# Kernel optimization log

Measured on AMD Instinct MI355X. Metric: run time of the kernel, lower is better.

Reference implementation:

```python
import jax, jax.numpy as jnp
import numpy as np

N, F_IN, HEADS, F_OUT = 4096, 128, 4, 32
DENSITY = 0.05


def setup_inputs() -> dict:
    key = jax.random.key(0)
    k_x, k_adj, k_w, k_as, k_ad, k_b = jax.random.split(key, 6)
    x = jax.random.normal(k_x, (N, F_IN), dtype=jnp.float32)
    # binary adjacency with self-loops so every row of Tau_sum is nonzero
    adj = (jax.random.uniform(k_adj, (N, N)) < DENSITY).astype(jnp.float32)
    adj = jnp.maximum(adj, jnp.eye(N, dtype=jnp.float32))
    weight = jax.random.normal(k_w, (HEADS * F_OUT, F_IN), dtype=jnp.float32) * 0.1
    att_src = jax.random.normal(k_as, (1, HEADS, F_OUT), dtype=jnp.float32) * 0.1
    att_dst = jax.random.normal(k_ad, (1, HEADS, F_OUT), dtype=jnp.float32) * 0.1
    bias = jax.random.normal(k_b, (HEADS * F_OUT,), dtype=jnp.float32) * 0.1
    return {"x": x, "adj_matrix": adj, "weight": weight,
            "att_src": att_src, "att_dst": att_dst, "bias": bias}


def reference(x, adj_matrix, weight, att_src, att_dst, bias):
    n = x.shape[0]
    heads = att_src.shape[1]
    f_out = weight.shape[0] // heads
    # H' = x W^T, reshaped to [N, heads, F_out]
    h_prime = (x @ weight.T).reshape(n, heads, f_out)
    alpha_src = jnp.sum(h_prime * att_src, axis=-1)  # [N, heads]
    alpha_dst = jnp.sum(h_prime * att_dst, axis=-1)  # [N, heads]
    # C[m, n, h] = alpha_src[n, h] + alpha_dst[m, h]
    C = alpha_src[None, :, :] + alpha_dst[:, None, :]
    adj_t = adj_matrix.T[..., None]                  # [N, N, 1]
    # exp(leaky_relu(C, 0.2)) masked by adjacency
    tau = adj_t * jnp.exp(jnp.maximum(0.2 * C, C))   # [N, N, heads]
    tau_sum = jnp.sum(tau, axis=1, keepdims=True)    # [N, 1, heads]
    att_weights = tau / tau_sum
    # Z[m, h, f] = sum_n (adjT * att)[m, n, h] * H'[n, h, f]
    z = jnp.einsum('mnh,nhf->mhf', adj_t * att_weights, h_prime)
    return z.reshape(n, heads * f_out) + bias
```

## Files before the change

kernel.cpp:

```cpp
#include <hip/hip_runtime.h>

#define N_NODES 4096
#define F_IN    128
#define HEADS   4
#define FTOT    128
#define CAP     512
#define LCAP    40

__global__ __launch_bounds__(128)
void k_hp(const float* __restrict__ x, const float* __restrict__ W,
          const float* __restrict__ att_src, const float* __restrict__ att_dst,
          float* __restrict__ hp, float* __restrict__ as_, float* __restrict__ ad_,
          int* __restrict__ cnt)
{
    const int b  = blockIdx.x;
    const int t  = threadIdx.x;
    const int i0 = b * 4;
    if (t < 4) cnt[i0 + t] = 0;
    __shared__ float xs[4 * F_IN];
    reinterpret_cast<float4*>(xs)[t] =
        reinterpret_cast<const float4*>(x + (size_t)i0 * F_IN)[t];
    __syncthreads();

    const float4* W4  = reinterpret_cast<const float4*>(W + t * F_IN);
    const float4* xs4 = reinterpret_cast<const float4*>(xs);
    float a0 = 0.f, a1 = 0.f, a2 = 0.f, a3 = 0.f;
#pragma unroll
    for (int k = 0; k < F_IN / 4; ++k) {
        const float4 w  = W4[k];
        const float4 v0 = xs4[k], v1 = xs4[32 + k], v2 = xs4[64 + k], v3 = xs4[96 + k];
        a0 = fmaf(w.x, v0.x, a0); a0 = fmaf(w.y, v0.y, a0); a0 = fmaf(w.z, v0.z, a0); a0 = fmaf(w.w, v0.w, a0);
        a1 = fmaf(w.x, v1.x, a1); a1 = fmaf(w.y, v1.y, a1); a1 = fmaf(w.z, v1.z, a1); a1 = fmaf(w.w, v1.w, a1);
        a2 = fmaf(w.x, v2.x, a2); a2 = fmaf(w.y, v2.y, a2); a2 = fmaf(w.z, v2.z, a2); a2 = fmaf(w.w, v2.w, a2);
        a3 = fmaf(w.x, v3.x, a3); a3 = fmaf(w.y, v3.y, a3); a3 = fmaf(w.z, v3.z, a3); a3 = fmaf(w.w, v3.w, a3);
    }
    hp[(size_t)(i0 + 0) * FTOT + t] = a0;
    hp[(size_t)(i0 + 1) * FTOT + t] = a1;
    hp[(size_t)(i0 + 2) * FTOT + t] = a2;
    hp[(size_t)(i0 + 3) * FTOT + t] = a3;

    const float asv = att_src[t], adv = att_dst[t];
    float s0 = a0 * asv, s1 = a1 * asv, s2 = a2 * asv, s3 = a3 * asv;
    float d0 = a0 * adv, d1 = a1 * adv, d2 = a2 * adv, d3 = a3 * adv;
#pragma unroll
    for (int s = 16; s; s >>= 1) {
        s0 += __shfl_xor(s0, s); s1 += __shfl_xor(s1, s);
        s2 += __shfl_xor(s2, s); s3 += __shfl_xor(s3, s);
        d0 += __shfl_xor(d0, s); d1 += __shfl_xor(d1, s);
        d2 += __shfl_xor(d2, s); d3 += __shfl_xor(d3, s);
    }
    if ((t & 31) == 0) {
        const int hh = t >> 5;
        as_[(i0 + 0) * HEADS + hh] = s0; as_[(i0 + 1) * HEADS + hh] = s1;
        as_[(i0 + 2) * HEADS + hh] = s2; as_[(i0 + 3) * HEADS + hh] = s3;
        ad_[(i0 + 0) * HEADS + hh] = d0; ad_[(i0 + 1) * HEADS + hh] = d1;
        ad_[(i0 + 2) * HEADS + hh] = d2; ad_[(i0 + 3) * HEADS + hh] = d3;
    }
}

__global__ __launch_bounds__(256)
void k_scan(const float* __restrict__ adj, int* __restrict__ cnt,
            unsigned short* __restrict__ lists)
{
    __shared__ int lcnt[64];
    __shared__ int gbase[64];
    __shared__ unsigned short lbuf[64][LCAP];
    const int t     = threadIdx.x;
    const int strip = blockIdx.x & 63;
    const int chunk = blockIdx.x >> 6;
    const int c0    = strip * 64;
    const int r0    = chunk * 128;
    const int q     = t & 15;
    const int p     = t >> 4;
    if (t < 64) lcnt[t] = 0;
    __syncthreads();

    const float4* adj4 = reinterpret_cast<const float4*>(adj);
    float4 v[8];
#pragma unroll
    for (int it = 0; it < 8; ++it)
        v[it] = adj4[(size_t)(r0 + p + it * 16) * (N_NODES / 4) + (c0 >> 2) + q];

    unsigned mk0 = 0, mk1 = 0, mk2 = 0, mk3 = 0;
#pragma unroll
    for (int it = 0; it < 8; ++it) {
        mk0 |= (v[it].x != 0.f) ? (1u << it) : 0u;
        mk1 |= (v[it].y != 0.f) ? (1u << it) : 0u;
        mk2 |= (v[it].z != 0.f) ? (1u << it) : 0u;
        mk3 |= (v[it].w != 0.f) ? (1u << it) : 0u;
    }
    unsigned mks[4] = {mk0, mk1, mk2, mk3};
#pragma unroll
    for (int j = 0; j < 4; ++j) {
        unsigned mask = mks[j];
        if (mask) {
            const int ml = 4 * q + j;
            int slot = atomicAdd(&lcnt[ml], __popc(mask));
            while (mask) {
                const int it = __ffs(mask) - 1;
                mask &= mask - 1;
                lbuf[ml][slot++] = (unsigned short)(r0 + p + it * 16);
            }
        }
    }
    __syncthreads();
    if (t < 64) gbase[t] = atomicAdd(&cnt[c0 + t], lcnt[t]);
    __syncthreads();
    const int ml  = t >> 2;
    const int sub = t & 3;
    const int nn  = lcnt[ml];
    unsigned short* dst = lists + (size_t)(c0 + ml) * CAP + gbase[ml];
    for (int j = sub; j < nn; j += 4) dst[j] = lbuf[ml][j];
}

__global__ __launch_bounds__(256)
void k_agg(const float* __restrict__ hp, const float* __restrict__ as_,
           const float* __restrict__ ad_, const int* __restrict__ cnt,
           const unsigned short* __restrict__ lists,
           const float* __restrict__ bias, float* __restrict__ out)
{
    __shared__ float e_s[4][64][4];
    __shared__ float mrg[2][32][5];
    const int t    = threadIdx.x;
    const int wv   = t >> 6;
    const int ms   = wv >> 1;
    const int wp   = wv & 1;
    const int l    = t & 63;
    const int m    = blockIdx.x * 2 + ms;
    const int half = l >> 5;
    const int l32  = l & 31;
    const int h    = l32 >> 3;

    const int2 c2   = reinterpret_cast<const int2*>(cnt)[blockIdx.x];
    const int  cm   = ms ? c2.y : c2.x;
    const int  chalf = (cm + 1) >> 1;
    const int  begin = wp ? chalf : 0;
    const int  end   = wp ? cm : chalf;

    const float4 adm = reinterpret_cast<const float4*>(ad_)[m];
    const unsigned short* lst = lists + (size_t)m * CAP;
    const float4* hp4 = reinterpret_cast<const float4*>(hp);
    const float4* as4 = reinterpret_cast<const float4*>(as_);

    float4 acc = make_float4(0.f, 0.f, 0.f, 0.f);
    float tau = 0.f;

    const int nbat = (end - begin + 63) >> 6;
    for (int b = 0; b < nbat; ++b) {
        const int k0 = begin + b * 64;
        const bool valid = (k0 + l) < end;
        const int myidx = valid ? (int)lst[k0 + l] : 0;
        const float4 a = as4[myidx];
        float4 e4;
        const float cx = a.x + adm.x, cy = a.y + adm.y, cz = a.z + adm.z, cw = a.w + adm.w;
        e4.x = valid ? __expf(fmaxf(0.2f * cx, cx)) : 0.f;
        e4.y = valid ? __expf(fmaxf(0.2f * cy, cy)) : 0.f;
        e4.z = valid ? __expf(fmaxf(0.2f * cz, cz)) : 0.f;
        e4.w = valid ? __expf(fmaxf(0.2f * cw, cw)) : 0.f;
        *reinterpret_cast<float4*>(&e_s[wv][l][0]) = e4;
        __builtin_amdgcn_wave_barrier();

        const int rem   = min(64, end - k0);
        const int pairs = (rem + 1) >> 1;
#pragma unroll 8
        for (int j = 0; j < pairs; ++j) {
            const int src = 2 * j + half;
            const int n   = __shfl(myidx, src);
            const float e = e_s[wv][src][h];
            const float4 hv = hp4[(size_t)n * (FTOT / 4) + l32];
            acc.x = fmaf(e, hv.x, acc.x);
            acc.y = fmaf(e, hv.y, acc.y);
            acc.z = fmaf(e, hv.z, acc.z);
            acc.w = fmaf(e, hv.w, acc.w);
            tau += e;
        }
    }

    acc.x += __shfl_xor(acc.x, 32);
    acc.y += __shfl_xor(acc.y, 32);
    acc.z += __shfl_xor(acc.z, 32);
    acc.w += __shfl_xor(acc.w, 32);
    tau   += __shfl_xor(tau, 32);

    if (wp == 1 && half == 0) {
        mrg[ms][l32][0] = acc.x; mrg[ms][l32][1] = acc.y;
        mrg[ms][l32][2] = acc.z; mrg[ms][l32][3] = acc.w;
        mrg[ms][l32][4] = tau;
    }
    __syncthreads();
    if (wp == 0 && half == 0) {
        acc.x += mrg[ms][l32][0]; acc.y += mrg[ms][l32][1];
        acc.z += mrg[ms][l32][2]; acc.w += mrg[ms][l32][3];
        tau   += mrg[ms][l32][4];
        const float inv = 1.f / tau;
        const float4 bv = reinterpret_cast<const float4*>(bias)[l32];
        float4 o;
        o.x = acc.x * inv + bv.x; o.y = acc.y * inv + bv.y;
        o.z = acc.z * inv + bv.z; o.w = acc.w * inv + bv.w;
        reinterpret_cast<float4*>(out)[(size_t)m * (FTOT / 4) + l32] = o;
    }
}

extern "C" void kernel_launch(void* const* d_in, const int* in_sizes, int n_in,
                              void* d_out, int out_size, void* d_ws, size_t ws_size,
                              hipStream_t stream) {
    const float* x       = (const float*)d_in[0];
    const float* adj     = (const float*)d_in[1];
    const float* weight  = (const float*)d_in[2];
    const float* att_src = (const float*)d_in[3];
    const float* att_dst = (const float*)d_in[4];
    const float* bias    = (const float*)d_in[5];
    float* out = (float*)d_out;

    float* ws  = (float*)d_ws;
    float* hp  = ws;
    float* as_ = hp  + (size_t)N_NODES * FTOT;
    float* ad_ = as_ + (size_t)N_NODES * HEADS;
    int*   cnt = (int*)(ad_ + (size_t)N_NODES * HEADS);
    unsigned short* lists = (unsigned short*)(cnt + N_NODES);

    k_hp  <<<N_NODES / 4, 128, 0, stream>>>(x, weight, att_src, att_dst, hp, as_, ad_, cnt);
    k_scan<<<2048, 256, 0, stream>>>(adj, cnt, lists);
    k_agg <<<N_NODES / 2, 256, 0, stream>>>(hp, as_, ad_, cnt, lists, bias, out);
}
```

Measured before the change: 52.75 us.

## Fuse projection and adjacency scan into one kernel; store projected features as bf16

Merges the feature projection and the adjacency-scan kernels into a single launch, with disjoint block ranges doing each job. The count reset moves to a memset so the scan blocks need not wait on the projection. Projected features are stored as bf16, halving the gather traffic in aggregation. Scan blocks now cover 256 rows each with a larger local buffer. The bf16 storage lowers the precision of the aggregated features, and the extra memset adds a launch.

Measured after the change: 51.67 us. -2.0%, faster.

```diff
diff --git a/kernel.cpp b/kernel.cpp
--- a/kernel.cpp
+++ b/kernel.cpp
@@ -1,120 +1,122 @@
 #include <hip/hip_runtime.h>
+#include <hip/hip_bf16.h>
 
 #define N_NODES 4096
 #define F_IN    128
 #define HEADS   4
 #define FTOT    128
 #define CAP     512
-#define LCAP    40
-
-__global__ __launch_bounds__(128)
-void k_hp(const float* __restrict__ x, const float* __restrict__ W,
-          const float* __restrict__ att_src, const float* __restrict__ att_dst,
-          float* __restrict__ hp, float* __restrict__ as_, float* __restrict__ ad_,
-          int* __restrict__ cnt)
+#define LCAP    48
+#define HPB     512
+#define SCB     1024
+
+__global__ __launch_bounds__(256)
+void k_pre(const float* __restrict__ x, const float* __restrict__ W,
+           const float* __restrict__ att_src, const float* __restrict__ att_dst,
+           const float* __restrict__ adj,
+           __hip_bfloat16* __restrict__ hpb, float* __restrict__ as_,
+           float* __restrict__ ad_, int* __restrict__ cnt,
+           unsigned short* __restrict__ lists)
 {
-    const int b  = blockIdx.x;
-    const int t  = threadIdx.x;
-    const int i0 = b * 4;
-    if (t < 4) cnt[i0 + t] = 0;
-    __shared__ float xs[4 * F_IN];
-    reinterpret_cast<float4*>(xs)[t] =
-        reinterpret_cast<const float4*>(x + (size_t)i0 * F_IN)[t];
-    __syncthreads();
-
-    const float4* W4  = reinterpret_cast<const float4*>(W + t * F_IN);
-    const float4* xs4 = reinterpret_cast<const float4*>(xs);
-    float a0 = 0.f, a1 = 0.f, a2 = 0.f, a3 = 0.f;
-#pragma unroll
-    for (int k = 0; k < F_IN / 4; ++k) {
-        const float4 w  = W4[k];
-        const float4 v0 = xs4[k], v1 = xs4[32 + k], v2 = xs4[64 + k], v3 = xs4[96 + k];
-        a0 = fmaf(w.x, v0.x, a0); a0 = fmaf(w.y, v0.y, a0); a0 = fmaf(w.z, v0.z, a0); a0 = fmaf(w.w, v0.w, a0);
-        a1 = fmaf(w.x, v1.x, a1); a1 = fmaf(w.y, v1.y, a1); a1 = fmaf(w.z, v1.z, a1); a1 = fmaf(w.w, v1.w, a1);
-        a2 = fmaf(w.x, v2.x, a2); a2 = fmaf(w.y, v2.y, a2); a2 = fmaf(w.z, v2.z, a2); a2 = fmaf(w.w, v2.w, a2);
-        a3 = fmaf(w.x, v3.x, a3); a3 = fmaf(w.y, v3.y, a3); a3 = fmaf(w.z, v3.z, a3); a3 = fmaf(w.w, v3.w, a3);
-    }
-    hp[(size_t)(i0 + 0) * FTOT + t] = a0;
-    hp[(size_t)(i0 + 1) * FTOT + t] = a1;
-    hp[(size_t)(i0 + 2) * FTOT + t] = a2;
-    hp[(size_t)(i0 + 3) * FTOT + t] = a3;
-
-    const float asv = att_src[t], adv = att_dst[t];
-    float s0 = a0 * asv, s1 = a1 * asv, s2 = a2 * asv, s3 = a3 * asv;
-    float d0 = a0 * adv, d1 = a1 * adv, d2 = a2 * adv, d3 = a3 * adv;
-#pragma unroll
-    for (int s = 16; s; s >>= 1) {
-        s0 += __shfl_xor(s0, s); s1 += __shfl_xor(s1, s);
-        s2 += __shfl_xor(s2, s); s3 += __shfl_xor(s3, s);
-        d0 += __shfl_xor(d0, s); d1 += __shfl_xor(d1, s);
-        d2 += __shfl_xor(d2, s); d3 += __shfl_xor(d3, s);
-    }
-    if ((t & 31) == 0) {
-        const int hh = t >> 5;
-        as_[(i0 + 0) * HEADS + hh] = s0; as_[(i0 + 1) * HEADS + hh] = s1;
-        as_[(i0 + 2) * HEADS + hh] = s2; as_[(i0 + 3) * HEADS + hh] = s3;
-        ad_[(i0 + 0) * HEADS + hh] = d0; ad_[(i0 + 1) * HEADS + hh] = d1;
-        ad_[(i0 + 2) * HEADS + hh] = d2; ad_[(i0 + 3) * HEADS + hh] = d3;
+    const int t = threadIdx.x;
+    if (blockIdx.x < HPB) {
+        __shared__ float xs[8 * F_IN];
+        const int sub = t >> 7;
+        const int tt  = t & 127;
+        const int i0  = blockIdx.x * 8 + sub * 4;
+        reinterpret_cast<float4*>(xs)[t] =
+            reinterpret_cast<const float4*>(x + (size_t)blockIdx.x * 8 * F_IN)[t];
+        __syncthreads();
+
+        const float4* W4  = reinterpret_cast<const float4*>(W + tt * F_IN);
+        const float4* xs4 = reinterpret_cast<const float4*>(xs + sub * 4 * F_IN);
+        float a0 = 0.f, a1 = 0.f, a2 = 0.f, a3 = 0.f;
+#pragma unroll
+        for (int k = 0; k < F_IN / 4; ++k) {
+            const float4 w  = W4[k];
+            const float4 v0 = xs4[k], v1 = xs4[32 + k], v2 = xs4[64 + k], v3 = xs4[96 + k];
+            a0 = fmaf(w.x, v0.x, a0); a0 = fmaf(w.y, v0.y, a0); a0 = fmaf(w.z, v0.z, a0); a0 = fmaf(w.w, v0.w, a0);
+            a1 = fmaf(w.x, v1.x, a1); a1 = fmaf(w.y, v1.y, a1); a1 = fmaf(w.z, v1.z, a1); a1 = fmaf(w.w, v1.w, a1);
+            a2 = fmaf(w.x, v2.x, a2); a2 = fmaf(w.y, v2.y, a2); a2 = fmaf(w.z, v2.z, a2); a2 = fmaf(w.w, v2.w, a2);
+            a3 = fmaf(w.x, v3.x, a3); a3 = fmaf(w.y, v3.y, a3); a3 = fmaf(w.z, v3.z, a3); a3 = fmaf(w.w, v3.w, a3);
+        }
+        hpb[(size_t)(i0 + 0) * FTOT + tt] = __float2bfloat16(a0);
+        hpb[(size_t)(i0 + 1) * FTOT + tt] = __float2bfloat16(a1);
+        hpb[(size_t)(i0 + 2) * FTOT + tt] = __float2bfloat16(a2);
+        hpb[(size_t)(i0 + 3) * FTOT + tt] = __float2bfloat16(a3);
+
+        const float asv = att_src[tt], adv = att_dst[tt];
+        float s0 = a0 * asv, s1 = a1 * asv, s2 = a2 * asv, s3 = a3 * asv;
+        float d0 = a0 * adv, d1 = a1 * adv, d2 = a2 * adv, d3 = a3 * adv;
+#pragma unroll
+        for (int s = 16; s; s >>= 1) {
+            s0 += __shfl_xor(s0, s); s1 += __shfl_xor(s1, s);
+            s2 += __shfl_xor(s2, s); s3 += __shfl_xor(s3, s);
+            d0 += __shfl_xor(d0, s); d1 += __shfl_xor(d1, s);
+            d2 += __shfl_xor(d2, s); d3 += __shfl_xor(d3, s);
+        }
+        if ((tt & 31) == 0) {
+            const int hh = tt >> 5;
+            as_[(i0 + 0) * HEADS + hh] = s0; as_[(i0 + 1) * HEADS + hh] = s1;
+            as_[(i0 + 2) * HEADS + hh] = s2; as_[(i0 + 3) * HEADS + hh] = s3;
+            ad_[(i0 + 0) * HEADS + hh] = d0; ad_[(i0 + 1) * HEADS + hh] = d1;
+            ad_[(i0 + 2) * HEADS + hh] = d2; ad_[(i0 + 3) * HEADS + hh] = d3;
+        }
+    } else {
+        __shared__ int lcnt[64];
+        __shared__ int gbase[64];
+        __shared__ unsigned short lbuf[64][LCAP];
+        const int sblk  = blockIdx.x - HPB;
+        const int strip = sblk & 63;
+        const int chunk = sblk >> 6;
+        const int c0    = strip * 64;
+        const int r0    = chunk * 256;
+        const int q     = t & 15;
+        const int p     = t >> 4;
+        if (t < 64) lcnt[t] = 0;
+        __syncthreads();
+
+        const float4* adj4 = reinterpret_cast<const float4*>(adj);
+        float4 v[16];
+#pragma unroll
+        for (int it = 0; it < 16; ++it)
+            v[it] = adj4[(size_t)(r0 + p + it * 16) * (N_NODES / 4) + (c0 >> 2) + q];
+
+        unsigned mk0 = 0, mk1 = 0, mk2 = 0, mk3 = 0;
+#pragma unroll
+        for (int it = 0; it < 16; ++it) {
+            mk0 |= (v[it].x != 0.f) ? (1u << it) : 0u;
+            mk1 |= (v[it].y != 0.f) ? (1u << it) : 0u;
+            mk2 |= (v[it].z != 0.f) ? (1u << it) : 0u;
+            mk3 |= (v[it].w != 0.f) ? (1u << it) : 0u;
+        }
+        unsigned mks[4] = {mk0, mk1, mk2, mk3};
+#pragma unroll
+        for (int j = 0; j < 4; ++j) {
+            unsigned mask = mks[j];
+            if (mask) {
+                const int ml = 4 * q + j;
+                int slot = atomicAdd(&lcnt[ml], __popc(mask));
+                while (mask) {
+                    const int it = __ffs(mask) - 1;
+                    mask &= mask - 1;
+                    lbuf[ml][slot++] = (unsigned short)(r0 + p + it * 16);
+                }
+            }
+        }
+        __syncthreads();
+        if (t < 64) gbase[t] = atomicAdd(&cnt[c0 + t], lcnt[t]);
+        __syncthreads();
+        const int ml  = t >> 2;
+        const int sub = t & 3;
+        const int nn  = lcnt[ml];
+        unsigned short* dst = lists + (size_t)(c0 + ml) * CAP + gbase[ml];
+        for (int j = sub; j < nn; j += 4) dst[j] = lbuf[ml][j];
     }
 }
 
 __global__ __launch_bounds__(256)
-void k_scan(const float* __restrict__ adj, int* __restrict__ cnt,
-            unsigned short* __restrict__ lists)
-{
-    __shared__ int lcnt[64];
-    __shared__ int gbase[64];
-    __shared__ unsigned short lbuf[64][LCAP];
-    const int t     = threadIdx.x;
-    const int strip = blockIdx.x & 63;
-    const int chunk = blockIdx.x >> 6;
-    const int c0    = strip * 64;
-    const int r0    = chunk * 128;
-    const int q     = t & 15;
-    const int p     = t >> 4;
-    if (t < 64) lcnt[t] = 0;
-    __syncthreads();
-
-    const float4* adj4 = reinterpret_cast<const float4*>(adj);
-    float4 v[8];
-#pragma unroll
-    for (int it = 0; it < 8; ++it)
-        v[it] = adj4[(size_t)(r0 + p + it * 16) * (N_NODES / 4) + (c0 >> 2) + q];
-
-    unsigned mk0 = 0, mk1 = 0, mk2 = 0, mk3 = 0;
-#pragma unroll
-    for (int it = 0; it < 8; ++it) {
-        mk0 |= (v[it].x != 0.f) ? (1u << it) : 0u;
-        mk1 |= (v[it].y != 0.f) ? (1u << it) : 0u;
-        mk2 |= (v[it].z != 0.f) ? (1u << it) : 0u;
-        mk3 |= (v[it].w != 0.f) ? (1u << it) : 0u;
-    }
-    unsigned mks[4] = {mk0, mk1, mk2, mk3};
-#pragma unroll
-    for (int j = 0; j < 4; ++j) {
-        unsigned mask = mks[j];
-        if (mask) {
-            const int ml = 4 * q + j;
-            int slot = atomicAdd(&lcnt[ml], __popc(mask));
-            while (mask) {
-                const int it = __ffs(mask) - 1;
-                mask &= mask - 1;
-                lbuf[ml][slot++] = (unsigned short)(r0 + p + it * 16);
-            }
-        }
-    }
-    __syncthreads();
-    if (t < 64) gbase[t] = atomicAdd(&cnt[c0 + t], lcnt[t]);
-    __syncthreads();
-    const int ml  = t >> 2;
-    const int sub = t & 3;
-    const int nn  = lcnt[ml];
-    unsigned short* dst = lists + (size_t)(c0 + ml) * CAP + gbase[ml];
-    for (int j = sub; j < nn; j += 4) dst[j] = lbuf[ml][j];
-}
-
-__global__ __launch_bounds__(256)
-void k_agg(const float* __restrict__ hp, const float* __restrict__ as_,
+void k_agg(const unsigned* __restrict__ hpw, const float* __restrict__ as_,
            const float* __restrict__ ad_, const int* __restrict__ cnt,
            const unsigned short* __restrict__ lists,
            const float* __restrict__ bias, float* __restrict__ out)
@@ -131,15 +133,15 @@
     const int l32  = l & 31;
     const int h    = l32 >> 3;
 
-    const int2 c2   = reinterpret_cast<const int2*>(cnt)[blockIdx.x];
-    const int  cm   = ms ? c2.y : c2.x;
+    const int2 c2    = reinterpret_cast<const int2*>(cnt)[blockIdx.x];
+    const int  cm    = ms ? c2.y : c2.x;
     const int  chalf = (cm + 1) >> 1;
     const int  begin = wp ? chalf : 0;
     const int  end   = wp ? cm : chalf;
 
     const float4 adm = reinterpret_cast<const float4*>(ad_)[m];
     const unsigned short* lst = lists + (size_t)m * CAP;
-    const float4* hp4 = reinterpret_cast<const float4*>(hp);
+    const uint2* hp2 = reinterpret_cast<const uint2*>(hpw);
     const float4* as4 = reinterpret_cast<const float4*>(as_);
 
     float4 acc = make_float4(0.f, 0.f, 0.f, 0.f);
@@ -167,11 +169,15 @@
             const int src = 2 * j + half;
             const int n   = __shfl(myidx, src);
             const float e = e_s[wv][src][h];
-            const float4 hv = hp4[(size_t)n * (FTOT / 4) + l32];
-            acc.x = fmaf(e, hv.x, acc.x);
-            acc.y = fmaf(e, hv.y, acc.y);
-            acc.z = fmaf(e, hv.z, acc.z);
-            acc.w = fmaf(e, hv.w, acc.w);
+            const uint2 u = hp2[(size_t)n * (FTOT / 4) + l32];
+            const float f0 = __uint_as_float(u.x << 16);
+            const float f1 = __uint_as_float(u.x & 0xffff0000u);
+            const float f2 = __uint_as_float(u.y << 16);
+            const float f3 = __uint_as_float(u.y & 0xffff0000u);
+            acc.x = fmaf(e, f0, acc.x);
+            acc.y = fmaf(e, f1, acc.y);
+            acc.z = fmaf(e, f2, acc.z);
+            acc.w = fmaf(e, f3, acc.w);
             tau += e;
         }
     }
@@ -212,14 +218,15 @@
     const float* bias    = (const float*)d_in[5];
     float* out = (float*)d_out;
 
-    float* ws  = (float*)d_ws;
-    float* hp  = ws;
-    float* as_ = hp  + (size_t)N_NODES * FTOT;
+    __hip_bfloat16* hpb = (__hip_bfloat16*)d_ws;
+    float* as_ = (float*)(hpb + (size_t)N_NODES * FTOT);
     float* ad_ = as_ + (size_t)N_NODES * HEADS;
     int*   cnt = (int*)(ad_ + (size_t)N_NODES * HEADS);
     unsigned short* lists = (unsigned short*)(cnt + N_NODES);
 
-    k_hp  <<<N_NODES / 4, 128, 0, stream>>>(x, weight, att_src, att_dst, hp, as_, ad_, cnt);
-    k_scan<<<2048, 256, 0, stream>>>(adj, cnt, lists);
-    k_agg <<<N_NODES / 2, 256, 0, stream>>>(hp, as_, ad_, cnt, lists, bias, out);
+    hipMemsetAsync(cnt, 0, N_NODES * sizeof(int), stream);
+    k_pre<<<HPB + SCB, 256, 0, stream>>>(x, weight, att_src, att_dst, adj,
+                                         hpb, as_, ad_, cnt, lists);
+    k_agg<<<N_NODES / 2, 256, 0, stream>>>((const unsigned*)hpb, as_, ad_, cnt,
+                                           lists, bias, out);
 }
```
